# Performance work log

Measured on AMD Instinct MI355X. Metric: run time of the kernel, lower is better.

The kernel has to match this reference:

```python
import jax, jax.numpy as jnp
import numpy as np

B, NP, K = 4, 8192, 16  # 4 point clouds of 8192 points, k=16 neighbors
C_IN = 16
FILTERS = [16, 32, 32]


def _knn(pos_b, k):
    # pos_b: [Np, 3] -> [Np, k] indices of k nearest (incl. self)
    sq = jnp.sum(pos_b * pos_b, axis=-1)  # [Np]
    d = sq[:, None] - 2.0 * (pos_b @ pos_b.T) + sq[None, :]  # [Np, Np]
    _, idx = jax.lax.top_k(-d, k)
    return idx


def _edge_conv(x, idx, W, b):
    # x: [B, Np, C]; idx: [B, Np, K] -> [B, Np, C_out]
    xj = jax.vmap(lambda xb, ib: xb[ib])(x, idx)          # gather: [B, Np, K, C]
    xi = x[:, :, None, :]                                  # [B, Np, 1, C]
    e = jnp.concatenate([jnp.broadcast_to(xi, xj.shape), xj - xi], axis=-1)  # [B,Np,K,2C]
    h = jax.nn.relu(jnp.einsum('bnkc,cd->bnkd', e, W) + b)
    return jnp.max(h, axis=2)                              # max-aggregate over neighbors


def setup_inputs() -> dict:
    key = jax.random.key(0)
    ks = jax.random.split(key, 8)
    xyz = jax.random.normal(ks[0], (B * NP, 3), dtype=jnp.float32) * 20.0
    bidx = jnp.repeat(jnp.arange(B, dtype=jnp.float32), NP)[:, None]
    point_coords = jnp.concatenate([bidx, xyz], axis=-1)   # [N, 4]
    point_features = jax.random.normal(ks[1], (B * NP, C_IN), dtype=jnp.float32)
    chans = [C_IN] + FILTERS
    params = {}
    for i in range(3):
        cin, cout = chans[i], chans[i + 1]
        scale = 1.0 / np.sqrt(2 * cin)
        params[f'W{i+1}'] = jax.random.normal(ks[2 + i], (2 * cin, cout), dtype=jnp.float32) * scale
        params[f'b{i+1}'] = jnp.zeros((cout,), dtype=jnp.float32)
    return dict(point_coords=point_coords, point_features=point_features, **params)


def reference(point_coords, point_features, W1, b1, W2, b2, W3, b3):
    pos = point_coords[:, 1:4].reshape(B, NP, 3)
    idx = jax.vmap(lambda p: _knn(p, K))(pos)              # [B, Np, K]
    x = point_features.reshape(B, NP, C_IN)
    x = _edge_conv(x, idx, W1, b1)
    x = _edge_conv(x, idx, W2, b2)
    x = _edge_conv(x, idx, W3, b3)
    return x.reshape(B * NP, FILTERS[-1])                  # [N, 32]
```

## Files before the change

### kernel.cpp

```cpp
#include <hip/hip_runtime.h>
#include <math.h>

#define NPTS 32768
#define NP   8192
#define KNN  16
#define CSPLIT 16
#define CHUNK (NP / CSPLIT)
#define SEGCAP 12
#define NSLOT (CSPLIT * SEGCAP)
#define QPT 2
#define QBLK (256 * QPT)

__device__ __forceinline__ float dist2f(float qx, float qy, float qz, float sqi, float4 t) {
    float dot = fmaf(qz, t.z, fmaf(qy, t.y, qx * t.x));
    return fmaf(-2.0f, dot, sqi) + t.w;
}

__device__ __forceinline__ void insert_val(float (&bd)[16], float d) {
    bd[15] = fminf(bd[15], d);
#pragma unroll
    for (int j = 15; j > 0; --j) {
        float lo = fminf(bd[j], bd[j - 1]);
        float hi = fmaxf(bd[j], bd[j - 1]);
        bd[j - 1] = lo; bd[j] = hi;
    }
}

__global__ __launch_bounds__(256) void knn_bound_kernel(
    const float4* __restrict__ coords, float* __restrict__ pb2)
{
    __shared__ float4 tile[CHUNK];

    const int tid = threadIdx.x;
    const int qb  = blockIdx.x * QBLK;
    const int batch = qb / NP;
    const int cbase = batch * NP + blockIdx.y * CHUNK;

    for (int c = tid; c < CHUNK; c += 256) {
        float4 f = coords[cbase + c];
        float sq = fmaf(f.w, f.w, fmaf(f.z, f.z, f.y * f.y));
        tile[c] = make_float4(f.y, f.z, f.w, sq);
    }

    const int q0 = qb + tid, q1 = qb + 256 + tid;
    float4 qf0 = coords[q0];
    float4 qf1 = coords[q1];
    const float qx0 = qf0.y, qy0 = qf0.z, qz0 = qf0.w;
    const float qx1 = qf1.y, qy1 = qf1.z, qz1 = qf1.w;
    const float sqi0 = fmaf(qz0, qz0, fmaf(qy0, qy0, qx0 * qx0));
    const float sqi1 = fmaf(qz1, qz1, fmaf(qy1, qy1, qx1 * qx1));

    float a0 = INFINITY, a1 = INFINITY;
    float b0 = INFINITY, b1 = INFINITY;
    __syncthreads();

#pragma unroll 4
    for (int c = 0; c < CHUNK; ++c) {
        float4 t = tile[c];
        float d0 = dist2f(qx0, qy0, qz0, sqi0, t);
        float d1 = dist2f(qx1, qy1, qz1, sqi1, t);
        float t0 = fminf(a1, d0);
        a1 = fmaxf(a0, t0);
        a0 = fminf(a0, t0);
        float t1 = fminf(b1, d1);
        b1 = fmaxf(b0, t1);
        b0 = fminf(b0, t1);
    }
    *(float2*)&pb2[(q0 * CSPLIT + blockIdx.y) * 2] = make_float2(a0, a1);
    *(float2*)&pb2[(q1 * CSPLIT + blockIdx.y) * 2] = make_float2(b0, b1);
}

__global__ __launch_bounds__(256) void tau_init_kernel(
    const float* __restrict__ pb2, float* __restrict__ tau)
{
    const int q = blockIdx.x * 256 + threadIdx.x;
    const float4* row = (const float4*)(pb2 + (size_t)q * 2 * CSPLIT);

    float bd[16];
#pragma unroll
    for (int j = 0; j < 16; ++j) bd[j] = INFINITY;
#pragma unroll
    for (int v = 0; v < 8; ++v) {
        float4 f = row[v];
        insert_val(bd, f.x);
        insert_val(bd, f.y);
        insert_val(bd, f.z);
        insert_val(bd, f.w);
    }
    tau[q] = bd[15];
}

__global__ __launch_bounds__(256) void knn_filter_kernel(
    const float4* __restrict__ coords, const float* __restrict__ tau,
    int* __restrict__ pc, int* __restrict__ surv)
{
    __shared__ float4 tile[CHUNK];

    const int tid = threadIdx.x;
    const int qb  = blockIdx.x * QBLK;
    const int batch = qb / NP;
    const int cbase = batch * NP + blockIdx.y * CHUNK;

    for (int c = tid; c < CHUNK; c += 256) {
        float4 f = coords[cbase + c];
        float sq = fmaf(f.w, f.w, fmaf(f.z, f.z, f.y * f.y));
        tile[c] = make_float4(f.y, f.z, f.w, sq);
    }

    const int q0 = qb + tid, q1 = qb + 256 + tid;
    float4 qf0 = coords[q0];
    float4 qf1 = coords[q1];
    const float qx0 = qf0.y, qy0 = qf0.z, qz0 = qf0.w;
    const float qx1 = qf1.y, qy1 = qf1.z, qz1 = qf1.w;
    const float sqi0 = fmaf(qz0, qz0, fmaf(qy0, qy0, qx0 * qx0));
    const float sqi1 = fmaf(qz1, qz1, fmaf(qy1, qy1, qx1 * qx1));
    const float tq0 = tau[q0], tq1 = tau[q1];

    const size_t sb0 = (size_t)q0 * NSLOT + blockIdx.y * SEGCAP;
    const size_t sb1 = (size_t)q1 * NSLOT + blockIdx.y * SEGCAP;
    int cnt0 = 0, cnt1 = 0;
    __syncthreads();

#pragma unroll 4
    for (int c = 0; c < CHUNK; ++c) {
        float4 t = tile[c];
        float d0 = dist2f(qx0, qy0, qz0, sqi0, t);
        float d1 = dist2f(qx1, qy1, qz1, sqi1, t);
        if (d0 <= tq0) {
            surv[sb0 + (cnt0 < SEGCAP ? cnt0 : SEGCAP - 1)] = cbase + c;
            ++cnt0;
        }
        if (d1 <= tq1) {
            surv[sb1 + (cnt1 < SEGCAP ? cnt1 : SEGCAP - 1)] = cbase + c;
            ++cnt1;
        }
    }
    pc[q0 * CSPLIT + blockIdx.y] = cnt0;
    pc[q1 * CSPLIT + blockIdx.y] = cnt1;
}

__global__ __launch_bounds__(64) void knn_select_ac1_kernel(
    const float4* __restrict__ coords, const int* __restrict__ pc,
    const int* __restrict__ surv,
    const float* __restrict__ feat, const float* __restrict__ W1,
    const float* __restrict__ b1,
    int* __restrict__ knn, float* __restrict__ a1, float* __restrict__ c1)
{
    __shared__ float sd[NSLOT];
    __shared__ int   si[NSLOT];
    __shared__ int   spc[CSPLIT];
    __shared__ int   soff[CSPLIT];
    __shared__ int   outi[16];
    __shared__ float sx[16];

    const int lane = threadIdx.x;
    const int q    = blockIdx.x;

    float4 qf = coords[q];
    const float qx = qf.y, qy = qf.z, qz = qf.w;
    const float sqi = fmaf(qz, qz, fmaf(qy, qy, qx * qx));

    if (lane < CSPLIT) spc[lane] = pc[q * CSPLIT + lane];
    __syncthreads();

    bool over = false;
    int acc = 0;
#pragma unroll
    for (int s = 0; s < CSPLIT; ++s) {
        int c = spc[s];
        over |= (c > SEGCAP);
        if (lane == 0) soff[s] = acc;
        acc += c;
    }
    const int n = acc;
    __syncthreads();

    if (!over) {
#pragma unroll
        for (int b = 0; b < 3; ++b) {
            const int j = b * 64 + lane;
            const int seg = j / SEGCAP;
            const int o   = j - seg * SEGCAP;
            if (o < spc[seg]) {
                int id = surv[(size_t)q * NSLOT + j];
                float4 f = coords[id];
                float sq = fmaf(f.w, f.w, fmaf(f.z, f.z, f.y * f.y));
                float d = dist2f(qx, qy, qz, sqi, make_float4(f.y, f.z, f.w, sq));
                const int pos = soff[seg] + o;
                sd[pos] = d; si[pos] = id;
            }
        }
        __syncthreads();

        if (n <= 64) {
            float dm = INFINITY; int im = 0x7fffffff;
            if (lane < n) { dm = sd[lane]; im = si[lane]; }
            int r = 0;
            for (int k = 0; k < n; ++k) {
                float dk = sd[k]; int ik = si[k];
                r += ((dk < dm) || (dk == dm && ik < im)) ? 1 : 0;
            }
            if (lane < n && r < 16) outi[r] = im;
        } else {
            float dm[3]; int im[3];
#pragma unroll
            for (int b = 0; b < 3; ++b) {
                const int m = b * 64 + lane;
                dm[b] = (m < n) ? sd[m] : INFINITY;
                im[b] = (m < n) ? si[m] : 0x7fffffff;
            }
            int r0 = 0, r1 = 0, r2 = 0;
            for (int k = 0; k < n; ++k) {
                float dk = sd[k]; int ik = si[k];
                r0 += ((dk < dm[0]) || (dk == dm[0] && ik < im[0])) ? 1 : 0;
                r1 += ((dk < dm[1]) || (dk == dm[1] && ik < im[1])) ? 1 : 0;
                r2 += ((dk < dm[2]) || (dk == dm[2] && ik < im[2])) ? 1 : 0;
            }
            if (lane       < n && r0 < 16) outi[r0] = im[0];
            if (lane + 64  < n && r1 < 16) outi[r1] = im[1];
            if (lane + 128 < n && r2 < 16) outi[r2] = im[2];
        }
        __syncthreads();
    } else {
        const int b0 = (q / NP) * NP;
        float lastd = -INFINITY; int lasti = -1;
        for (int r = 0; r < 16; ++r) {
            float md = INFINITY; int mi = 0x7fffffff;
            for (int c = lane; c < NP; c += 64) {
                int id = b0 + c;
                float4 f = coords[id];
                float sq = fmaf(f.w, f.w, fmaf(f.z, f.z, f.y * f.y));
                float d = dist2f(qx, qy, qz, sqi, make_float4(f.y, f.z, f.w, sq));
                bool gt_last = (d > lastd) || (d == lastd && id > lasti);
                bool lt_min  = (d < md) || (d == md && id < mi);
                if (gt_last && lt_min) { md = d; mi = id; }
            }
#pragma unroll
            for (int s = 1; s < 64; s <<= 1) {
                float od = __shfl_xor(md, s);
                int   oi = __shfl_xor(mi, s);
                bool less = (od < md) || (od == md && oi < mi);
                md = less ? od : md;
                mi = less ? oi : mi;
            }
            if (lane == 0) outi[r] = mi;
            lastd = md; lasti = mi;
        }
        __syncthreads();
    }

    if (lane < 16) {
        knn[q * 16 + lane] = outi[lane];
        sx[lane] = feat[(size_t)q * 16 + lane];
    }
    __syncthreads();

    if (lane < 16) {
        float av = b1[lane], cv = 0.0f;
#pragma unroll
        for (int r = 0; r < 16; ++r) {
            float xr = sx[r];
            float wt = W1[r * 16 + lane];
            float wb = W1[(16 + r) * 16 + lane];
            av = fmaf(xr, wt - wb, av);
            cv = fmaf(xr, wb, cv);
        }
        a1[(size_t)q * 16 + lane] = av;
        c1[(size_t)q * 16 + lane] = cv;
    }
}

template<int COUT, int CNXT, bool LAST>
__global__ __launch_bounds__(256) void edgeconv_kernel(
    const float* __restrict__ a, const float* __restrict__ cf,
    const int* __restrict__ knn,
    const float* __restrict__ Wn, const float* __restrict__ bn,
    float* __restrict__ an, float* __restrict__ cn, float* __restrict__ out)
{
    constexpr int CPG  = COUT / 4;
    constexpr int CPGN = LAST ? 4 : CNXT / 4;
    constexpr int WSZ  = LAST ? 1 : COUT * CNXT;

    __shared__ float xs[64][COUT + 1];
    __shared__ __align__(16) float wm[WSZ];
    __shared__ __align__(16) float wb[WSZ];

    const int tid = threadIdx.x;
    const int g = tid & 3, p = tid >> 2;
    const int i = blockIdx.x * 64 + p;

    if constexpr (!LAST) {
        for (int t = tid; t < COUT * CNXT; t += 256) {
            float top = Wn[t], bot = Wn[COUT * CNXT + t];
            wm[t] = top - bot; wb[t] = bot;
        }
    }

    float av[CPG], m[CPG];
    const float4* a4 = (const float4*)(a + (size_t)i * COUT + g * CPG);
#pragma unroll
    for (int v = 0; v < CPG / 4; ++v) {
        float4 f = a4[v];
        av[4*v] = f.x; av[4*v+1] = f.y; av[4*v+2] = f.z; av[4*v+3] = f.w;
    }
#pragma unroll
    for (int c = 0; c < CPG; ++c) m[c] = -INFINITY;

    const int4* kn = (const int4*)(knn + (size_t)i * 16);
#pragma unroll
    for (int kk = 0; kk < 4; ++kk) {
        int4 n4 = kn[kk];
        int js[4] = { n4.x, n4.y, n4.z, n4.w };
#pragma unroll
        for (int u = 0; u < 4; ++u) {
            const float4* c4 = (const float4*)(cf + (size_t)js[u] * COUT + g * CPG);
#pragma unroll
            for (int v = 0; v < CPG / 4; ++v) {
                float4 f = c4[v];
                m[4*v+0] = fmaxf(m[4*v+0], av[4*v+0] + f.x);
                m[4*v+1] = fmaxf(m[4*v+1], av[4*v+1] + f.y);
                m[4*v+2] = fmaxf(m[4*v+2], av[4*v+2] + f.z);
                m[4*v+3] = fmaxf(m[4*v+3], av[4*v+3] + f.w);
            }
        }
    }
    float xv[CPG];
#pragma unroll
    for (int c = 0; c < CPG; ++c) xv[c] = fmaxf(m[c], 0.0f);

    if constexpr (LAST) {
        float4* o4 = (float4*)(out + (size_t)i * COUT + g * CPG);
#pragma unroll
        for (int v = 0; v < CPG / 4; ++v)
            o4[v] = make_float4(xv[4*v], xv[4*v+1], xv[4*v+2], xv[4*v+3]);
    } else {
#pragma unroll
        for (int c = 0; c < CPG; ++c) xs[p][g * CPG + c] = xv[c];
        __syncthreads();

        float aacc[CPGN], cacc[CPGN];
        const float4* bn4 = (const float4*)(bn + g * CPGN);
#pragma unroll
        for (int v = 0; v < CPGN / 4; ++v) {
            float4 f = bn4[v];
            aacc[4*v] = f.x; aacc[4*v+1] = f.y; aacc[4*v+2] = f.z; aacc[4*v+3] = f.w;
        }
#pragma unroll
        for (int c = 0; c < CPGN; ++c) cacc[c] = 0.0f;

#pragma unroll
        for (int r = 0; r < COUT; ++r) {
            float xr = xs[p][r];
            const float4* wm4 = (const float4*)(wm + r * CNXT + g * CPGN);
            const float4* wb4 = (const float4*)(wb + r * CNXT + g * CPGN);
#pragma unroll
            for (int v = 0; v < CPGN / 4; ++v) {
                float4 fm = wm4[v], fb = wb4[v];
                aacc[4*v+0] = fmaf(xr, fm.x, aacc[4*v+0]);
                aacc[4*v+1] = fmaf(xr, fm.y, aacc[4*v+1]);
                aacc[4*v+2] = fmaf(xr, fm.z, aacc[4*v+2]);
                aacc[4*v+3] = fmaf(xr, fm.w, aacc[4*v+3]);
                cacc[4*v+0] = fmaf(xr, fb.x, cacc[4*v+0]);
                cacc[4*v+1] = fmaf(xr, fb.y, cacc[4*v+1]);
                cacc[4*v+2] = fmaf(xr, fb.z, cacc[4*v+2]);
                cacc[4*v+3] = fmaf(xr, fb.w, cacc[4*v+3]);
            }
        }
        float4* an4 = (float4*)(an + (size_t)i * CNXT + g * CPGN);
        float4* cn4 = (float4*)(cn + (size_t)i * CNXT + g * CPGN);
#pragma unroll
        for (int v = 0; v < CPGN / 4; ++v) {
            an4[v] = make_float4(aacc[4*v], aacc[4*v+1], aacc[4*v+2], aacc[4*v+3]);
            cn4[v] = make_float4(cacc[4*v], cacc[4*v+1], cacc[4*v+2], cacc[4*v+3]);
        }
    }
}

extern "C" void kernel_launch(void* const* d_in, const int* in_sizes, int n_in,
                              void* d_out, int out_size, void* d_ws, size_t ws_size,
                              hipStream_t stream) {
    const float4* coords = (const float4*)d_in[0];
    const float*  feat   = (const float*)d_in[1];
    const float*  W1 = (const float*)d_in[2];
    const float*  b1 = (const float*)d_in[3];
    const float*  W2 = (const float*)d_in[4];
    const float*  b2 = (const float*)d_in[5];
    const float*  W3 = (const float*)d_in[6];
    const float*  b3 = (const float*)d_in[7];
    float* out = (float*)d_out;

    char* ws = (char*)d_ws;
    int*   surv = (int*)  (ws);
    float* pb2  = (float*)(ws + (24u << 20));
    float* tau  = (float*)(ws + (28u << 20));
    int*   pc   = (int*)  (ws + (29u << 20));
    int*   knn  = (int*)  (ws + (31u << 20));
    float* a1   = (float*)(ws + (33u << 20));
    float* c1   = (float*)(ws + (35u << 20));
    float* a2   = (float*)(ws + (0u  << 20));
    float* c2   = (float*)(ws + (4u  << 20));
    float* a3   = (float*)(ws + (8u  << 20));
    float* c3   = (float*)(ws + (12u << 20));

    knn_bound_kernel<<<dim3(NPTS / QBLK, CSPLIT), 256, 0, stream>>>(coords, pb2);
    tau_init_kernel<<<NPTS / 256, 256, 0, stream>>>(pb2, tau);
    knn_filter_kernel<<<dim3(NPTS / QBLK, CSPLIT), 256, 0, stream>>>(coords, tau, pc, surv);
    knn_select_ac1_kernel<<<NPTS, 64, 0, stream>>>(coords, pc, surv, feat, W1, b1, knn, a1, c1);
    edgeconv_kernel<16, 32, false><<<NPTS / 64, 256, 0, stream>>>(a1, c1, knn, W2, b2, a2, c2, nullptr);
    edgeconv_kernel<32, 32, false><<<NPTS / 64, 256, 0, stream>>>(a2, c2, knn, W3, b3, a3, c3, nullptr);
    edgeconv_kernel<32, 4, true><<<NPTS / 64, 256, 0, stream>>>(a3, c3, knn, nullptr, nullptr, nullptr, nullptr, out);
}
```

Baseline: 244.3 us.

## Double candidate chunk split and transpose per-chunk bound buffer layout

Raises the number of candidate chunks per query from 16 to 32, halving chunk size and per-chunk survivor capacity, so the bound and filter kernels launch twice as many blocks for more parallelism. The per-chunk two-smallest bound buffer is stored transposed (chunk-major, query-minor) so stores and the tau_init reads are coalesced. The workspace layout is reshuffled, with knn now aliasing the bound buffer. Tau is now the 16th smallest of 64 per-chunk bounds, which is looser, and the smaller segment capacity of 6 survivors per chunk may overflow more often.

```diff
diff --git a/kernel.cpp b/kernel.cpp
--- a/kernel.cpp
+++ b/kernel.cpp
@@ -4,9 +4,9 @@
 #define NPTS 32768
 #define NP   8192
 #define KNN  16
-#define CSPLIT 16
+#define CSPLIT 32
 #define CHUNK (NP / CSPLIT)
-#define SEGCAP 12
+#define SEGCAP 6
 #define NSLOT (CSPLIT * SEGCAP)
 #define QPT 2
 #define QBLK (256 * QPT)
@@ -27,7 +27,7 @@
 }
 
 __global__ __launch_bounds__(256) void knn_bound_kernel(
-    const float4* __restrict__ coords, float* __restrict__ pb2)
+    const float4* __restrict__ coords, float* __restrict__ pb2T)
 {
     __shared__ float4 tile[CHUNK];
 
@@ -36,10 +36,10 @@
     const int batch = qb / NP;
     const int cbase = batch * NP + blockIdx.y * CHUNK;
 
-    for (int c = tid; c < CHUNK; c += 256) {
-        float4 f = coords[cbase + c];
+    {
+        float4 f = coords[cbase + tid];
         float sq = fmaf(f.w, f.w, fmaf(f.z, f.z, f.y * f.y));
-        tile[c] = make_float4(f.y, f.z, f.w, sq);
+        tile[tid] = make_float4(f.y, f.z, f.w, sq);
     }
 
     const int q0 = qb + tid, q1 = qb + 256 + tid;
@@ -66,27 +66,23 @@
         b1 = fmaxf(b0, t1);
         b0 = fminf(b0, t1);
     }
-    *(float2*)&pb2[(q0 * CSPLIT + blockIdx.y) * 2] = make_float2(a0, a1);
-    *(float2*)&pb2[(q1 * CSPLIT + blockIdx.y) * 2] = make_float2(b0, b1);
+    const size_t r0 = (size_t)(blockIdx.y * 2) * NPTS;
+    const size_t r1 = r0 + NPTS;
+    pb2T[r0 + q0] = a0; pb2T[r1 + q0] = a1;
+    pb2T[r0 + q1] = b0; pb2T[r1 + q1] = b1;
 }
 
 __global__ __launch_bounds__(256) void tau_init_kernel(
-    const float* __restrict__ pb2, float* __restrict__ tau)
+    const float* __restrict__ pb2T, float* __restrict__ tau)
 {
     const int q = blockIdx.x * 256 + threadIdx.x;
-    const float4* row = (const float4*)(pb2 + (size_t)q * 2 * CSPLIT);
 
     float bd[16];
 #pragma unroll
     for (int j = 0; j < 16; ++j) bd[j] = INFINITY;
 #pragma unroll
-    for (int v = 0; v < 8; ++v) {
-        float4 f = row[v];
-        insert_val(bd, f.x);
-        insert_val(bd, f.y);
-        insert_val(bd, f.z);
-        insert_val(bd, f.w);
-    }
+    for (int v = 0; v < 2 * CSPLIT; ++v)
+        insert_val(bd, pb2T[(size_t)v * NPTS + q]);
     tau[q] = bd[15];
 }
 
@@ -101,10 +97,10 @@
     const int batch = qb / NP;
     const int cbase = batch * NP + blockIdx.y * CHUNK;
 
-    for (int c = tid; c < CHUNK; c += 256) {
-        float4 f = coords[cbase + c];
+    {
+        float4 f = coords[cbase + tid];
         float sq = fmaf(f.w, f.w, fmaf(f.z, f.z, f.y * f.y));
-        tile[c] = make_float4(f.y, f.z, f.w, sq);
+        tile[tid] = make_float4(f.y, f.z, f.w, sq);
     }
 
     const int q0 = qb + tid, q1 = qb + 256 + tid;
@@ -391,19 +387,19 @@
 
     char* ws = (char*)d_ws;
     int*   surv = (int*)  (ws);
-    float* pb2  = (float*)(ws + (24u << 20));
-    float* tau  = (float*)(ws + (28u << 20));
-    int*   pc   = (int*)  (ws + (29u << 20));
-    int*   knn  = (int*)  (ws + (31u << 20));
-    float* a1   = (float*)(ws + (33u << 20));
-    float* c1   = (float*)(ws + (35u << 20));
+    float* pb2T = (float*)(ws + (24u << 20));
+    int*   knn  = (int*)  (ws + (24u << 20));
+    float* a1   = (float*)(ws + (26u << 20));
+    float* c1   = (float*)(ws + (28u << 20));
+    int*   pc   = (int*)  (ws + (30u << 20));
+    float* tau  = (float*)(ws + (34u << 20));
     float* a2   = (float*)(ws + (0u  << 20));
     float* c2   = (float*)(ws + (4u  << 20));
     float* a3   = (float*)(ws + (8u  << 20));
     float* c3   = (float*)(ws + (12u << 20));
 
-    knn_bound_kernel<<<dim3(NPTS / QBLK, CSPLIT), 256, 0, stream>>>(coords, pb2);
-    tau_init_kernel<<<NPTS / 256, 256, 0, stream>>>(pb2, tau);
+    knn_bound_kernel<<<dim3(NPTS / QBLK, CSPLIT), 256, 0, stream>>>(coords, pb2T);
+    tau_init_kernel<<<NPTS / 256, 256, 0, stream>>>(pb2T, tau);
     knn_filter_kernel<<<dim3(NPTS / QBLK, CSPLIT), 256, 0, stream>>>(coords, tau, pc, surv);
     knn_select_ac1_kernel<<<NPTS, 64, 0, stream>>>(coords, pc, surv, feat, W1, b1, knn, a1, c1);
     edgeconv_kernel<16, 32, false><<<NPTS / 64, 256, 0, stream>>>(a1, c1, knn, W2, b2, a2, c2, nullptr);
```

After: 645.3 us. +164.1%, slower.
